# Performance work log

Hardware: AMD Instinct MI355X
Metric: run time of the kernel (lower is better)

## Reference

```python
import jax, jax.numpy as jnp
import numpy as np

NB, NA, NC, NH, NW = 16, 5, 80, 64, 64
MAXT = 50            # max gt boxes per image
THRESH = 0.6         # ignore threshold
NOOBJ_SCALE = 1.0
OBJ_SCALE = 5.0
NTOT = NB * NA * NH * NW


def _iou_cwh(b1, b2):
    """IoU for center-format (x,y,w,h) boxes, broadcasting over leading dims."""
    x1, y1, w1, h1 = (b1[..., i] for i in range(4))
    x2, y2, w2, h2 = (b2[..., i] for i in range(4))
    cw = jnp.minimum(x1 + 0.5 * w1, x2 + 0.5 * w2) - jnp.maximum(x1 - 0.5 * w1, x2 - 0.5 * w2)
    ch = jnp.minimum(y1 + 0.5 * h1, y2 + 0.5 * h2) - jnp.maximum(y1 - 0.5 * h1, y2 - 0.5 * h2)
    inter = jnp.maximum(cw, 0.0) * jnp.maximum(ch, 0.0)
    union = w1 * h1 + w2 * h2 - inter
    return jnp.where(inter > 0, inter / union, 0.0)


def setup_inputs() -> dict:
    key = jax.random.key(0)
    k1, k2, k3, k4 = jax.random.split(key, 4)
    output = jax.random.normal(k1, (NB, NA * (5 + NC), NH, NW), jnp.float32)
    nval = 20  # valid boxes per image; rest zero (loop-break semantics)
    cls = jax.random.randint(k2, (NB, nval), 0, NC).astype(jnp.float32)
    xy = jax.random.uniform(k3, (NB, nval, 2), minval=0.05, maxval=0.95)
    wh = jax.random.uniform(k4, (NB, nval, 2), minval=0.05, maxval=0.30)
    boxes = jnp.concatenate([cls[..., None], xy, wh], axis=-1)      # [NB,nval,5]
    pad = jnp.zeros((NB, MAXT - nval, 5), jnp.float32)
    target = jnp.concatenate([boxes, pad], axis=1).reshape(NB, MAXT * 5)
    anchors = jnp.array([[0.57273, 0.677385], [1.87446, 2.06253], [3.33843, 5.47434],
                         [7.88282, 3.52778], [9.77052, 9.16828]], jnp.float32)
    return {"output": output, "target": target, "anchors": anchors}


def reference(output, target, anchors):
    target = jax.lax.stop_gradient(target)  # target.detach() in torch
    out = output.reshape(NB, NA, 5 + NC, NH, NW)
    tx = jax.nn.sigmoid(out[:, :, 0])
    ty = jax.nn.sigmoid(out[:, :, 1])
    tw, th = out[:, :, 2], out[:, :, 3]
    conf = jax.nn.sigmoid(out[:, :, 4])                   # [B,A,H,W]
    cls_logits = jnp.moveaxis(out[:, :, 5:], 2, -1)       # [B,A,H,W,C]

    aw, ah = anchors[:, 0], anchors[:, 1]
    # decoded pred boxes, detached (only used for target building, as in torch)
    pred = jax.lax.stop_gradient(jnp.stack([
        tx + jnp.arange(NW, dtype=jnp.float32)[None, None, None, :],
        ty + jnp.arange(NH, dtype=jnp.float32)[None, None, :, None],
        jnp.exp(tw) * aw[None, :, None, None],
        jnp.exp(th) * ah[None, :, None, None]], axis=-1))  # [B,A,H,W,4]
    anchors_sg = jax.lax.stop_gradient(anchors)
    aw_sg, ah_sg = anchors_sg[:, 0], anchors_sg[:, 1]

    tb = target.reshape(NB, MAXT, 5)
    # torch breaks at first box with x==0 -> cumulative validity
    valid = jnp.cumprod((tb[:, :, 1] != 0).astype(jnp.int32), axis=1) > 0  # [B,T]
    gcls = tb[:, :, 0]
    gx, gw = tb[:, :, 1] * NW, tb[:, :, 3] * NW
    gy, gh = tb[:, :, 2] * NH, tb[:, :, 4] * NH
    gt = jnp.stack([gx, gy, gw, gh], axis=-1)             # [B,T,4]

    # ignore mask: max IoU of each pred box against all valid gt
    ious = _iou_cwh(gt[:, :, None, None, None, :], pred[:, None])  # [B,T,A,H,W]
    ious = jnp.where(valid[:, :, None, None, None], ious, 0.0)
    conf_mask = jnp.where(ious.max(axis=1) > THRESH, 0.0, NOOBJ_SCALE)  # [B,A,H,W]

    # anchor assignment: IoU of (0,0,gw,gh) vs (0,0,aw,ah) -> argmax anchor
    inter = jnp.minimum(gw[..., None], aw_sg) * jnp.minimum(gh[..., None], ah_sg)
    union = gw[..., None] * gh[..., None] + aw_sg * ah_sg - inter
    best_n = jnp.argmax(inter / union, axis=-1)           # [B,T]

    gi = jnp.clip(gx.astype(jnp.int32), 0, NW - 1)
    gj = jnp.clip(gy.astype(jnp.int32), 0, NH - 1)
    cell = best_n * (NH * NW) + gj * NW + gi              # [B,T] index in A*H*W
    mpred = jnp.take_along_axis(pred.reshape(NB, NA * NH * NW, 4), cell[:, :, None], axis=1)
    iou_best = _iou_cwh(gt, mpred)                        # [B,T]

    flat = cell + jnp.arange(NB)[:, None] * (NA * NH * NW)
    flat = jnp.where(valid, flat, NTOT).reshape(-1)       # out-of-range -> dropped
    fv = lambda v: v.reshape(-1)
    gw_s = jnp.where(valid, gw, 1.0)
    gh_s = jnp.where(valid, gh, 1.0)
    awb, ahb = aw_sg[best_n], ah_sg[best_n]

    cls_mask = jnp.zeros(NTOT, jnp.float32).at[flat].set(1.0, mode='drop')
    conf_mask = conf_mask.reshape(-1).at[flat].set(OBJ_SCALE, mode='drop')
    # seen < 12800 -> tcoord xy default 0.5, coord_mask all ones
    t0 = jnp.full((NTOT,), 0.5).at[flat].set(fv(gx - gi.astype(jnp.float32)), mode='drop')
    t1 = jnp.full((NTOT,), 0.5).at[flat].set(fv(gy - gj.astype(jnp.float32)), mode='drop')
    t2 = jnp.zeros(NTOT).at[flat].set(fv(jnp.log(gw_s / awb)), mode='drop')
    t3 = jnp.zeros(NTOT).at[flat].set(fv(jnp.log(gh_s / ahb)), mode='drop')
    tconf = jnp.zeros(NTOT).at[flat].set(fv(iou_best), mode='drop')
    tcls = jnp.zeros(NTOT, jnp.int32).at[flat].set(fv(gcls.astype(jnp.int32)), mode='drop')

    coord = jnp.stack([tx, ty, tw, th], axis=0).reshape(4, NTOT)
    tcoord = jnp.stack([t0, t1, t2, t3], axis=0)
    loss_coord = 0.5 * jnp.sum((coord - tcoord) ** 2)     # coord_mask == 1 everywhere
    loss_conf = 0.5 * jnp.sum(conf_mask * (conf.reshape(-1) - tconf) ** 2)
    logp = jax.nn.log_softmax(cls_logits, axis=-1).reshape(NTOT, NC)
    ce = -jnp.take_along_axis(logp, tcls[:, None], axis=1)[:, 0]
    loss_cls = jnp.sum(ce * cls_mask)
    return loss_coord + loss_conf + loss_cls
```

## Files before the change

### kernel.cpp

```cpp
#include <hip/hip_runtime.h>
#include <math.h>

constexpr int kNB   = 16;
constexpr int kNA   = 5;
constexpr int kNC   = 80;
constexpr int kNH   = 64;
constexpr int kNW   = 64;
constexpr int kMAXT = 50;
constexpr int kCH    = 5 + kNC;
constexpr int kPLANE = kNH * kNW;
constexpr int kCELLS_B = kNA * kPLANE;
constexpr int kBLK  = 256;
constexpr int kBPB  = kCELLS_B / kBLK;
constexpr int kGRID = kNB * kBPB;
constexpr float kOBJ = 5.0f;

constexpr int kRECF = 16;

__device__ __forceinline__ float frcp(float x) { return __builtin_amdgcn_rcpf(x); }
__device__ __forceinline__ float fsig(float x) { return frcp(1.0f + __expf(-x)); }

__global__ __launch_bounds__(256) void k_fused(const float* __restrict__ out,
                                               const float* __restrict__ target,
                                               const float* __restrict__ anchors,
                                               float* __restrict__ partials) {
    __shared__ __align__(16) float srec[kMAXT * kRECF];
    __shared__ int snv;
    __shared__ float wred[4];

    const int tid  = threadIdx.x;
    const int b    = blockIdx.x / kBPB;
    const int t_ce = blockIdx.x % kBPB;

    if (tid < 64) {
        int t = tid;
        float c0 = 0.f, x = 0.f, y = 0.f, w = 0.f, h = 0.f;
        if (t < kMAXT) {
            const float* tp = target + (b * kMAXT + t) * 5;
            c0 = tp[0]; x = tp[1]; y = tp[2]; w = tp[3]; h = tp[4];
        }
        unsigned long long m = __ballot(x != 0.0f);
        int nv = (int)__builtin_ctzll(~m);
        if (t == 0) snv = nv;

        bool act = (t < nv);
        int cell = -1, gi = 0, gj = 0, bn = 0;
        float gx = 0, gy = 0, gw = 0, gh = 0, aw = 1.f, ah = 1.f;
        if (act) {
            gx = x * kNW; gy = y * kNH; gw = w * kNW; gh = h * kNH;
            float best = -1.0f;
            for (int n = 0; n < kNA; ++n) {
                float aw_ = anchors[2 * n], ah_ = anchors[2 * n + 1];
                float inter = fminf(gw, aw_) * fminf(gh, ah_);
                float uni = gw * gh + aw_ * ah_ - inter;
                float r = inter / uni;
                if (r > best) { best = r; bn = n; }
            }
            aw = anchors[2 * bn]; ah = anchors[2 * bn + 1];
            gi = (int)gx; gi = gi < 0 ? 0 : (gi > kNW - 1 ? kNW - 1 : gi);
            gj = (int)gy; gj = gj < 0 ? 0 : (gj > kNH - 1 ? kNH - 1 : gj);
            cell = bn * kPLANE + gj * kNW + gi;
        }
        bool owner = act;
        for (int t2 = 0; t2 < kMAXT; ++t2) {
            int c2 = __shfl(cell, t2, 64);
            if (act && t2 > t && t2 < nv && c2 == cell) owner = false;
        }
        if (act) {
            const float* ob = out + ((size_t)(b * kNA + bn) * kCH) * kPLANE + gj * kNW + gi;
            float px = fsig(ob[0]) + (float)gi;
            float py = fsig(ob[kPLANE]) + (float)gj;
            float pw = __expf(ob[2 * kPLANE]) * aw;
            float ph = __expf(ob[3 * kPLANE]) * ah;
            float cw  = fminf(gx + 0.5f * gw, px + 0.5f * pw) - fmaxf(gx - 0.5f * gw, px - 0.5f * pw);
            float chh = fminf(gy + 0.5f * gh, py + 0.5f * ph) - fmaxf(gy - 0.5f * gh, py - 0.5f * ph);
            float inter = fmaxf(cw, 0.f) * fmaxf(chh, 0.f);
            float uni = gw * gh + pw * ph - inter;
            float iou = (inter > 0.f) ? inter / uni : 0.f;

            float* r = srec + t * kRECF;
            r[0]  = gx - 0.5f * gw;  r[1]  = gx + 0.5f * gw;
            r[2]  = gy - 0.5f * gh;  r[3]  = gy + 0.5f * gh;
            r[4]  = 0.6f * gw * gh;  r[5]  = __int_as_float(cell);
            r[6]  = 0.f;             r[7]  = 0.f;
            r[8]  = gx - (float)gi;  r[9]  = gy - (float)gj;
            r[10] = __logf(gw / aw); r[11] = __logf(gh / ah);
            r[12] = iou;             r[13] = c0;
            r[14] = owner ? 1.f : 0.f; r[15] = 0.f;
        }
    }
    __syncthreads();
    const int nv = snv;

    float ceV0 = 0.f, ceV1 = -INFINITY, ceLt = 0.f;
    bool doCE = false;
    if (tid < 64 && t_ce < nv && srec[t_ce * kRECF + 14] != 0.f) {
        doCE = true;
        int cell = __float_as_int(srec[t_ce * kRECF + 5]);
        int bn = cell >> 12, pix = cell & (kPLANE - 1);
        int tcls = (int)srec[t_ce * kRECF + 13];
        const float* lg = out + ((size_t)(b * kNA + bn) * kCH + 5) * kPLANE + pix;
        ceV0 = lg[(size_t)tid * kPLANE];
        if (tid < kNC - 64) ceV1 = lg[(size_t)(64 + tid) * kPLANE];
        ceLt = lg[(size_t)tcls * kPLANE];
    }

    int a = (t_ce * kBLK + tid) / kPLANE;
    int remp = (t_ce * kBLK + tid) & (kPLANE - 1);
    int i = remp & (kNW - 1), j = remp >> 6;

    const float* ob = out + ((size_t)(b * kNA + a) * kCH) * kPLANE + remp;
    float tx   = fsig(ob[0]);
    float ty   = fsig(ob[kPLANE]);
    float tw   = ob[2 * kPLANE];
    float th   = ob[3 * kPLANE];
    float conf = fsig(ob[4 * kPLANE]);

    float aw = anchors[2 * a], ah = anchors[2 * a + 1];
    float pw = __expf(tw) * aw, ph = __expf(th) * ah;
    float px = tx + (float)i, py = ty + (float)j;
    float px1 = px - 0.5f * pw, px2 = px + 0.5f * pw;
    float py1 = py - 0.5f * ph, py2 = py + 0.5f * ph;
    float p06 = 0.6f * pw * ph;
    int mycell = a * kPLANE + remp;

    float flag = -1.f;
    int match = -1;
    for (int t = 0; t < nv; ++t) {
        const float4 bx = *reinterpret_cast<const float4*>(srec + t * kRECF);
        const float2 gc = *reinterpret_cast<const float2*>(srec + t * kRECF + 4);
        float cw  = fminf(bx.y, px2) - fmaxf(bx.x, px1);
        float chh = fminf(bx.w, py2) - fmaxf(bx.z, py1);
        float inter = fmaxf(cw, 0.f) * fmaxf(chh, 0.f);
        flag = fmaxf(flag, fmaf(1.6f, inter, -(gc.x + p06)));
        match = (__float_as_int(gc.y) == mycell) ? t : match;
    }

    float t0 = 0.5f, t1 = 0.5f, t2 = 0.f, t3 = 0.f, tconf = 0.f, cmask;
    if (match >= 0) {
        const float4 tt = *reinterpret_cast<const float4*>(srec + match * kRECF + 8);
        t0 = tt.x; t1 = tt.y; t2 = tt.z; t3 = tt.w;
        tconf = srec[match * kRECF + 12];
        cmask = kOBJ;
    } else {
        cmask = (flag > 0.f) ? 0.f : 1.f;
    }

    float dx = tx - t0, dy = ty - t1, dw = tw - t2, dh = th - t3, dc = conf - tconf;
    float loss = 0.5f * (dx * dx + dy * dy + dw * dw + dh * dh)
               + 0.5f * cmask * dc * dc;

    if (doCE) {
        float mx = fmaxf(ceV0, ceV1);
        #pragma unroll
        for (int off = 32; off > 0; off >>= 1) mx = fmaxf(mx, __shfl_xor(mx, off, 64));
        float s = __expf(ceV0 - mx) + ((tid < kNC - 64) ? __expf(ceV1 - mx) : 0.f);
        #pragma unroll
        for (int off = 32; off > 0; off >>= 1) s += __shfl_xor(s, off, 64);
        if (tid == 0) loss += __logf(s) + mx - ceLt;
    }

    #pragma unroll
    for (int off = 32; off > 0; off >>= 1) loss += __shfl_down(loss, off, 64);
    if ((tid & 63) == 0) wred[tid >> 6] = loss;
    __syncthreads();
    if (tid == 0)
        partials[blockIdx.x] = wred[0] + wred[1] + wred[2] + wred[3];
}

__global__ __launch_bounds__(256) void k_final(const float* __restrict__ partials,
                                               float* __restrict__ outv) {
    __shared__ float red[256];
    float s = 0.f;
    for (int k = threadIdx.x; k < kGRID; k += 256) s += partials[k];
    red[threadIdx.x] = s;
    __syncthreads();
    for (int off = 128; off > 0; off >>= 1) {
        if (threadIdx.x < off) red[threadIdx.x] += red[threadIdx.x + off];
        __syncthreads();
    }
    if (threadIdx.x == 0) outv[0] = red[0];
}

extern "C" void kernel_launch(void* const* d_in, const int* in_sizes, int n_in,
                              void* d_out, int out_size, void* d_ws, size_t ws_size,
                              hipStream_t stream) {
    const float* output  = (const float*)d_in[0];
    const float* target  = (const float*)d_in[1];
    const float* anchors = (const float*)d_in[2];

    float* partials = (float*)d_ws;

    k_fused<<<kGRID, kBLK, 0, stream>>>(output, target, anchors, partials);
    k_final<<<1, 256, 0, stream>>>(partials, (float*)d_out);
}
```

Before: 17.13 us.

## Overlap box preprocessing and CE gather across waves, hoist cell loads

Issues each thread's five per-cell global loads before the prologue so their latency overlaps target preprocessing. Wave 1 now redundantly recomputes the gt cells, does duplicate-owner detection with a single ballot, and starts the class-logit gather before the barrier instead of after it. The per-box p06 term moves out of the inner IoU loop, and the final reduction shrinks to a single wave using shuffles. It adds duplicated prologue work in wave 1 and higher register pressure from the early loads.

```diff
diff --git a/kernel.cpp b/kernel.cpp
--- a/kernel.cpp
+++ b/kernel.cpp
@@ -29,11 +29,27 @@
     __shared__ float wred[4];
 
     const int tid  = threadIdx.x;
+    const int wave = tid >> 6;
+    const int lane = tid & 63;
     const int b    = blockIdx.x / kBPB;
     const int t_ce = blockIdx.x % kBPB;
 
-    if (tid < 64) {
-        int t = tid;
+    const int cidx = t_ce * kBLK + tid;
+    const int a    = cidx / kPLANE;
+    const int remp = cidx & (kPLANE - 1);
+    const int i    = remp & (kNW - 1), j = remp >> 6;
+    const float* ob = out + ((size_t)(b * kNA + a) * kCH) * kPLANE + remp;
+    float o0 = ob[0];
+    float o1 = ob[kPLANE];
+    float o2 = ob[2 * kPLANE];
+    float o3 = ob[3 * kPLANE];
+    float o4 = ob[4 * kPLANE];
+
+    float ceV0 = 0.f, ceV1 = -INFINITY, ceLt = 0.f;
+    bool doCE = false;
+
+    if (wave == 0) {
+        int t = lane;
         float c0 = 0.f, x = 0.f, y = 0.f, w = 0.f, h = 0.f;
         if (t < kMAXT) {
             const float* tp = target + (b * kMAXT + t) * 5;
@@ -43,12 +59,9 @@
         int nv = (int)__builtin_ctzll(~m);
         if (t == 0) snv = nv;
 
-        bool act = (t < nv);
-        int cell = -1, gi = 0, gj = 0, bn = 0;
-        float gx = 0, gy = 0, gw = 0, gh = 0, aw = 1.f, ah = 1.f;
-        if (act) {
-            gx = x * kNW; gy = y * kNH; gw = w * kNW; gh = h * kNH;
-            float best = -1.0f;
+        if (t < nv) {
+            float gx = x * kNW, gy = y * kNH, gw = w * kNW, gh = h * kNH;
+            int bn = 0; float best = -1.0f;
             for (int n = 0; n < kNA; ++n) {
                 float aw_ = anchors[2 * n], ah_ = anchors[2 * n + 1];
                 float inter = fminf(gw, aw_) * fminf(gh, ah_);
@@ -56,22 +69,16 @@
                 float r = inter / uni;
                 if (r > best) { best = r; bn = n; }
             }
-            aw = anchors[2 * bn]; ah = anchors[2 * bn + 1];
-            gi = (int)gx; gi = gi < 0 ? 0 : (gi > kNW - 1 ? kNW - 1 : gi);
-            gj = (int)gy; gj = gj < 0 ? 0 : (gj > kNH - 1 ? kNH - 1 : gj);
-            cell = bn * kPLANE + gj * kNW + gi;
-        }
-        bool owner = act;
-        for (int t2 = 0; t2 < kMAXT; ++t2) {
-            int c2 = __shfl(cell, t2, 64);
-            if (act && t2 > t && t2 < nv && c2 == cell) owner = false;
-        }
-        if (act) {
-            const float* ob = out + ((size_t)(b * kNA + bn) * kCH) * kPLANE + gj * kNW + gi;
-            float px = fsig(ob[0]) + (float)gi;
-            float py = fsig(ob[kPLANE]) + (float)gj;
-            float pw = __expf(ob[2 * kPLANE]) * aw;
-            float ph = __expf(ob[3 * kPLANE]) * ah;
+            float aw = anchors[2 * bn], ah = anchors[2 * bn + 1];
+            int gi = (int)gx; gi = gi < 0 ? 0 : (gi > kNW - 1 ? kNW - 1 : gi);
+            int gj = (int)gy; gj = gj < 0 ? 0 : (gj > kNH - 1 ? kNH - 1 : gj);
+            int cell = bn * kPLANE + gj * kNW + gi;
+
+            const float* mb = out + ((size_t)(b * kNA + bn) * kCH) * kPLANE + gj * kNW + gi;
+            float px = fsig(mb[0]) + (float)gi;
+            float py = fsig(mb[kPLANE]) + (float)gj;
+            float pw = __expf(mb[2 * kPLANE]) * aw;
+            float ph = __expf(mb[3 * kPLANE]) * ah;
             float cw  = fminf(gx + 0.5f * gw, px + 0.5f * pw) - fmaxf(gx - 0.5f * gw, px - 0.5f * pw);
             float chh = fminf(gy + 0.5f * gh, py + 0.5f * ph) - fmaxf(gy - 0.5f * gh, py - 0.5f * ph);
             float inter = fmaxf(cw, 0.f) * fmaxf(chh, 0.f);
@@ -82,39 +89,56 @@
             r[0]  = gx - 0.5f * gw;  r[1]  = gx + 0.5f * gw;
             r[2]  = gy - 0.5f * gh;  r[3]  = gy + 0.5f * gh;
             r[4]  = 0.6f * gw * gh;  r[5]  = __int_as_float(cell);
-            r[6]  = 0.f;             r[7]  = 0.f;
             r[8]  = gx - (float)gi;  r[9]  = gy - (float)gj;
             r[10] = __logf(gw / aw); r[11] = __logf(gh / ah);
             r[12] = iou;             r[13] = c0;
-            r[14] = owner ? 1.f : 0.f; r[15] = 0.f;
+        }
+    } else if (wave == 1) {
+        int t = lane;
+        float c0 = 0.f, x = 0.f, y = 0.f, w = 0.f, h = 0.f;
+        if (t < kMAXT) {
+            const float* tp = target + (b * kMAXT + t) * 5;
+            c0 = tp[0]; x = tp[1]; y = tp[2]; w = tp[3]; h = tp[4];
+        }
+        unsigned long long m = __ballot(x != 0.0f);
+        int nv = (int)__builtin_ctzll(~m);
+
+        int cell = -1;
+        if (t < nv) {
+            float gx = x * kNW, gy = y * kNH, gw = w * kNW, gh = h * kNH;
+            int bn = 0; float best = -1.0f;
+            for (int n = 0; n < kNA; ++n) {
+                float aw_ = anchors[2 * n], ah_ = anchors[2 * n + 1];
+                float inter = fminf(gw, aw_) * fminf(gh, ah_);
+                float uni = gw * gh + aw_ * ah_ - inter;
+                float r = inter / uni;
+                if (r > best) { best = r; bn = n; }
+            }
+            int gi = (int)gx; gi = gi < 0 ? 0 : (gi > kNW - 1 ? kNW - 1 : gi);
+            int gj = (int)gy; gj = gj < 0 ? 0 : (gj > kNH - 1 ? kNH - 1 : gj);
+            cell = bn * kPLANE + gj * kNW + gi;
+        }
+        int   cellT = __shfl(cell, t_ce & 63, 64);
+        float c0T   = __shfl(c0,   t_ce & 63, 64);
+        unsigned long long dup = __ballot(t > t_ce && cell == cellT && cell >= 0);
+        doCE = (t_ce < nv) && (dup == 0ull);
+        if (doCE) {
+            int bn = cellT >> 12, pix = cellT & (kPLANE - 1);
+            int tcls = (int)c0T;
+            const float* lg = out + ((size_t)(b * kNA + bn) * kCH + 5) * kPLANE + pix;
+            ceV0 = lg[(size_t)lane * kPLANE];
+            if (lane < kNC - 64) ceV1 = lg[(size_t)(64 + lane) * kPLANE];
+            ceLt = lg[(size_t)tcls * kPLANE];
         }
     }
     __syncthreads();
     const int nv = snv;
 
-    float ceV0 = 0.f, ceV1 = -INFINITY, ceLt = 0.f;
-    bool doCE = false;
-    if (tid < 64 && t_ce < nv && srec[t_ce * kRECF + 14] != 0.f) {
-        doCE = true;
-        int cell = __float_as_int(srec[t_ce * kRECF + 5]);
-        int bn = cell >> 12, pix = cell & (kPLANE - 1);
-        int tcls = (int)srec[t_ce * kRECF + 13];
-        const float* lg = out + ((size_t)(b * kNA + bn) * kCH + 5) * kPLANE + pix;
-        ceV0 = lg[(size_t)tid * kPLANE];
-        if (tid < kNC - 64) ceV1 = lg[(size_t)(64 + tid) * kPLANE];
-        ceLt = lg[(size_t)tcls * kPLANE];
-    }
-
-    int a = (t_ce * kBLK + tid) / kPLANE;
-    int remp = (t_ce * kBLK + tid) & (kPLANE - 1);
-    int i = remp & (kNW - 1), j = remp >> 6;
-
-    const float* ob = out + ((size_t)(b * kNA + a) * kCH) * kPLANE + remp;
-    float tx   = fsig(ob[0]);
-    float ty   = fsig(ob[kPLANE]);
-    float tw   = ob[2 * kPLANE];
-    float th   = ob[3 * kPLANE];
-    float conf = fsig(ob[4 * kPLANE]);
+    float tx   = fsig(o0);
+    float ty   = fsig(o1);
+    float tw   = o2;
+    float th   = o3;
+    float conf = fsig(o4);
 
     float aw = anchors[2 * a], ah = anchors[2 * a + 1];
     float pw = __expf(tw) * aw, ph = __expf(th) * ah;
@@ -124,7 +148,7 @@
     float p06 = 0.6f * pw * ph;
     int mycell = a * kPLANE + remp;
 
-    float flag = -1.f;
+    float flag = -INFINITY;
     int match = -1;
     for (int t = 0; t < nv; ++t) {
         const float4 bx = *reinterpret_cast<const float4*>(srec + t * kRECF);
@@ -132,7 +156,7 @@
         float cw  = fminf(bx.y, px2) - fmaxf(bx.x, px1);
         float chh = fminf(bx.w, py2) - fmaxf(bx.z, py1);
         float inter = fmaxf(cw, 0.f) * fmaxf(chh, 0.f);
-        flag = fmaxf(flag, fmaf(1.6f, inter, -(gc.x + p06)));
+        flag = fmaxf(flag, fmaf(1.6f, inter, -gc.x));
         match = (__float_as_int(gc.y) == mycell) ? t : match;
     }
 
@@ -143,43 +167,38 @@
         tconf = srec[match * kRECF + 12];
         cmask = kOBJ;
     } else {
-        cmask = (flag > 0.f) ? 0.f : 1.f;
+        cmask = (flag > p06) ? 0.f : 1.f;
     }
 
     float dx = tx - t0, dy = ty - t1, dw = tw - t2, dh = th - t3, dc = conf - tconf;
     float loss = 0.5f * (dx * dx + dy * dy + dw * dw + dh * dh)
                + 0.5f * cmask * dc * dc;
 
-    if (doCE) {
+    if (wave == 1 && doCE) {
         float mx = fmaxf(ceV0, ceV1);
         #pragma unroll
         for (int off = 32; off > 0; off >>= 1) mx = fmaxf(mx, __shfl_xor(mx, off, 64));
-        float s = __expf(ceV0 - mx) + ((tid < kNC - 64) ? __expf(ceV1 - mx) : 0.f);
+        float s = __expf(ceV0 - mx) + ((lane < kNC - 64) ? __expf(ceV1 - mx) : 0.f);
         #pragma unroll
         for (int off = 32; off > 0; off >>= 1) s += __shfl_xor(s, off, 64);
-        if (tid == 0) loss += __logf(s) + mx - ceLt;
+        if (lane == 0) loss += __logf(s) + mx - ceLt;
     }
 
     #pragma unroll
     for (int off = 32; off > 0; off >>= 1) loss += __shfl_down(loss, off, 64);
-    if ((tid & 63) == 0) wred[tid >> 6] = loss;
+    if (lane == 0) wred[wave] = loss;
     __syncthreads();
     if (tid == 0)
         partials[blockIdx.x] = wred[0] + wred[1] + wred[2] + wred[3];
 }
 
-__global__ __launch_bounds__(256) void k_final(const float* __restrict__ partials,
-                                               float* __restrict__ outv) {
-    __shared__ float red[256];
+__global__ __launch_bounds__(64) void k_final(const float* __restrict__ partials,
+                                              float* __restrict__ outv) {
     float s = 0.f;
-    for (int k = threadIdx.x; k < kGRID; k += 256) s += partials[k];
-    red[threadIdx.x] = s;
-    __syncthreads();
-    for (int off = 128; off > 0; off >>= 1) {
-        if (threadIdx.x < off) red[threadIdx.x] += red[threadIdx.x + off];
-        __syncthreads();
-    }
-    if (threadIdx.x == 0) outv[0] = red[0];
+    for (int k = threadIdx.x; k < kGRID; k += 64) s += partials[k];
+    #pragma unroll
+    for (int off = 32; off > 0; off >>= 1) s += __shfl_xor(s, off, 64);
+    if (threadIdx.x == 0) outv[0] = s;
 }
 
 extern "C" void kernel_launch(void* const* d_in, const int* in_sizes, int n_in,
@@ -192,5 +211,5 @@
     float* partials = (float*)d_ws;
 
     k_fused<<<kGRID, kBLK, 0, stream>>>(output, target, anchors, partials);
-    k_final<<<1, 256, 0, stream>>>(partials, (float*)d_out);
+    k_final<<<1, 64, 0, stream>>>(partials, (float*)d_out);
 }
```

Result: no change. 16.94 us (-1.1%).
